# Performance work log

Measured on AMD Instinct MI355X. Metric: run time of the kernel, lower is better.

Reference implementation:

```python
import jax, jax.numpy as jnp
import numpy as np

B, D, NH, NT = 4096, 2048, 16, 4
DK = D // NH
EPS = 1e-5


def setup_inputs() -> dict:
    key = jax.random.key(0)
    ks = jax.random.split(key, 16)
    s = 0.02
    inp = {
        "e0": jax.random.normal(ks[0], (B, D), jnp.float32),
        "e1": jax.random.normal(ks[1], (B, D), jnp.float32),
        "e2": jax.random.normal(ks[2], (B, D), jnp.float32),
        "e3": jax.random.normal(ks[3], (B, D), jnp.float32),
        "quality": jax.random.uniform(ks[4], (B, NT), jnp.float32),
        "Wq": jax.random.normal(ks[5], (D, D), jnp.float32) * s,
        "bq": jnp.zeros((D,), jnp.float32),
        "Wk": jax.random.normal(ks[6], (D, D), jnp.float32) * s,
        "bk": jnp.zeros((D,), jnp.float32),
        "Wv": jax.random.normal(ks[7], (D, D), jnp.float32) * s,
        "bv": jnp.zeros((D,), jnp.float32),
        "Wo": jax.random.normal(ks[8], (D, D), jnp.float32) * s,
        "bo": jnp.zeros((D,), jnp.float32),
        "gamma": jnp.ones((D,), jnp.float32),
        "beta": jnp.zeros((D,), jnp.float32),
    }
    return inp


def _layer_norm(x, gamma, beta):
    mu = jnp.mean(x, axis=-1, keepdims=True)
    var = jnp.mean(jnp.square(x - mu), axis=-1, keepdims=True)
    return (x - mu) * jax.lax.rsqrt(var + EPS) * gamma + beta


def reference(e0, e1, e2, e3, quality, Wq, bq, Wk, bk, Wv, bv, Wo, bo, gamma, beta):
    # H: (B, T=4, D) stacked evidence representations
    H = jnp.stack([e0, e1, e2, e3], axis=1)
    # QKV projections, reshaped to (B, heads, T, dk)
    def proj(W, b):
        return (jnp.einsum('btd,ed->bte', H, W) + b).reshape(B, NT, NH, DK).transpose(0, 2, 1, 3)
    Q, K, V = proj(Wq, bq), proj(Wk, bk), proj(Wv, bv)
    # scores: (B, heads, Tq, Tk), scaled then multiplicatively quality-gated on keys
    scores = jnp.einsum('bhid,bhjd->bhij', Q, K) / jnp.sqrt(jnp.float32(DK))
    scores = scores * quality[:, None, None, :]
    attn = jax.nn.softmax(scores, axis=-1)  # dropout = identity at inference
    ctx = jnp.einsum('bhij,bhjd->bhid', attn, V)          # (B, H, T, dk)
    ctx = ctx.transpose(0, 2, 1, 3).reshape(B, NT, D)      # (B, T, D)
    ctx = jnp.einsum('btd,ed->bte', ctx, Wo) + bo
    fused = jnp.mean(ctx, axis=1)       # mean over evidence types
    residual = jnp.mean(H, axis=1)      # mean of ALL evidence types
    return _layer_norm(fused + residual, gamma, beta)
```

## Files before the change

kernel.cpp:

```cpp
#include <hip/hip_runtime.h>
#include <cstdint>
#include <cstddef>

#define BB 4096
#define DD 2048
#define NHH 16
#define NTT 4
#define DKK 128

using u16 = unsigned short;
using u32 = unsigned int;

typedef __bf16 bf16x8 __attribute__((ext_vector_type(8)));
typedef float f32x4 __attribute__((ext_vector_type(4)));

__device__ __forceinline__ float b2f(u16 u) {
    union { float f; u32 i; } c; c.i = ((u32)u) << 16; return c.f;
}
__device__ __forceinline__ u16 f2b(float f) {
    union { float f; u32 i; } c; c.f = f;
    u32 x = c.i;
    u32 r = (x + 0x7fffu + ((x >> 16) & 1u)) >> 16;
    return (u16)r;
}
__device__ __forceinline__ u32 pk(float lo, float hi) {
    u32 a = __builtin_bit_cast(u32, lo) + 0x8000u;
    u32 b = __builtin_bit_cast(u32, hi) + 0x8000u;
    return __builtin_amdgcn_perm(b, a, 0x07060302u);
}

__device__ __forceinline__ void load_lds16(const void* g, void* l) {
    __builtin_amdgcn_global_load_lds((const __attribute__((address_space(1))) void*)g,
                                     (__attribute__((address_space(3))) void*)l,
                                     16, 0, 0);
}

__global__ __launch_bounds__(256) void cvt_all(
    const float* __restrict__ e0, const float* __restrict__ e1,
    const float* __restrict__ e2, const float* __restrict__ e3,
    const float* __restrict__ Wq, const float* __restrict__ Wk,
    const float* __restrict__ Wv, const float* __restrict__ Wo,
    u16* __restrict__ Ebf, u16* __restrict__ W4, float* __restrict__ resid)
{
    const int blk = blockIdx.x;
    const int tid = threadIdx.x;
    if (blk < 4096) {
        const int b = blk;
        const int c = tid * 8;
        const size_t rb = (size_t)b * DD + c;
        const float* eps[4] = {e0, e1, e2, e3};
        float a8[8] = {0, 0, 0, 0, 0, 0, 0, 0};
#pragma unroll
        for (int t = 0; t < 4; ++t) {
            float4 p0 = *(const float4*)(eps[t] + rb);
            float4 p1 = *(const float4*)(eps[t] + rb + 4);
            u16* dst = Ebf + ((size_t)(b * 4 + t)) * DD + c;
            *(uint4*)dst = make_uint4(pk(p0.x, p0.y), pk(p0.z, p0.w),
                                      pk(p1.x, p1.y), pk(p1.z, p1.w));
            a8[0] += p0.x; a8[1] += p0.y; a8[2] += p0.z; a8[3] += p0.w;
            a8[4] += p1.x; a8[5] += p1.y; a8[6] += p1.z; a8[7] += p1.w;
        }
        *(float4*)(resid + rb)     = make_float4(a8[0] * 0.25f, a8[1] * 0.25f,
                                                 a8[2] * 0.25f, a8[3] * 0.25f);
        *(float4*)(resid + rb + 4) = make_float4(a8[4] * 0.25f, a8[5] * 0.25f,
                                                 a8[6] * 0.25f, a8[7] * 0.25f);
    } else {
        const int wb = blk - 4096;
        const int w = wb >> 11;
        const float* src = (w == 0) ? Wq : (w == 1) ? Wk : (w == 2) ? Wv : Wo;
        u16* dst = W4 + (size_t)w * DD * DD;
        const size_t i = (size_t)(wb & 2047) * 2048 + tid * 8;
        float4 a = *(const float4*)(src + i);
        float4 c2 = *(const float4*)(src + i + 4);
        *(uint4*)(dst + i) = make_uint4(pk(a.x, a.y), pk(a.z, a.w),
                                        pk(c2.x, c2.y), pk(c2.z, c2.w));
    }
}

#define QKV_COMPUTE(BI)                                                        \
    {                                                                          \
        bf16x8 af[4];                                                          \
        _Pragma("unroll")                                                      \
        for (int mi = 0; mi < 4; ++mi)                                         \
            af[mi] = *(const bf16x8*)((const char*)As[BI] +                    \
                     (wm + mi * 16 + lrow) * 64 + soff);                       \
        {                                                                      \
            bf16x8 b4[4];                                                      \
            _Pragma("unroll")                                                  \
            for (int ni = 0; ni < 4; ++ni)                                     \
                b4[ni] = *(const bf16x8*)((const char*)BQs[BI] +               \
                         (wn + ni * 16 + lrow) * 64 + soff);                   \
            _Pragma("unroll")                                                  \
            for (int mi = 0; mi < 4; ++mi)                                     \
                _Pragma("unroll")                                              \
                for (int ni = 0; ni < 4; ++ni)                                 \
                    aQ[mi][ni] = __builtin_amdgcn_mfma_f32_16x16x32_bf16(      \
                        af[mi], b4[ni], aQ[mi][ni], 0, 0, 0);                  \
        }                                                                      \
        __builtin_amdgcn_sched_barrier(0);                                     \
        {                                                                      \
            bf16x8 b4[4];                                                      \
            _Pragma("unroll")                                                  \
            for (int ni = 0; ni < 4; ++ni)                                     \
                b4[ni] = *(const bf16x8*)((const char*)BKs[BI] +               \
                         (wn + ni * 16 + lrow) * 64 + soff);                   \
            _Pragma("unroll")                                                  \
            for (int mi = 0; mi < 4; ++mi)                                     \
                _Pragma("unroll")                                              \
                for (int ni = 0; ni < 4; ++ni)                                 \
                    aK[mi][ni] = __builtin_amdgcn_mfma_f32_16x16x32_bf16(      \
                        af[mi], b4[ni], aK[mi][ni], 0, 0, 0);                  \
        }                                                                      \
        __builtin_amdgcn_sched_barrier(0);                                     \
        {                                                                      \
            bf16x8 b4[4];                                                      \
            _Pragma("unroll")                                                  \
            for (int ni = 0; ni < 4; ++ni)                                     \
                b4[ni] = *(const bf16x8*)((const char*)BVs[BI] +               \
                         (wn + ni * 16 + lrow) * 64 + soff);                   \
            _Pragma("unroll")                                                  \
            for (int mi = 0; mi < 4; ++mi)                                     \
                _Pragma("unroll")                                              \
                for (int ni = 0; ni < 4; ++ni)                                 \
                    aV[mi][ni] = __builtin_amdgcn_mfma_f32_16x16x32_bf16(      \
                        af[mi], b4[ni], aV[mi][ni], 0, 0, 0);                  \
        }                                                                      \
        __builtin_amdgcn_sched_barrier(0);                                     \
    }

#define QKV_STAGE(BI, KT)                                                      \
    {                                                                          \
        const size_t ko = (size_t)(KT) * 32;                                   \
        char* dA = (char*)As[BI]  + wave * 1024;                               \
        char* dQ = (char*)BQs[BI] + wave * 1024;                               \
        char* dK = (char*)BKs[BI] + wave * 1024;                               \
        char* dV = (char*)BVs[BI] + wave * 1024;                               \
        load_lds16(srcA + ko, dA);       load_lds16(srcA + ko + D64, dA + 4096);\
        load_lds16(srcQ + ko, dQ);       load_lds16(srcQ + ko + D64, dQ + 4096);\
        load_lds16(srcK + ko, dK);       load_lds16(srcK + ko + D64, dK + 4096);\
        load_lds16(srcV + ko, dV);       load_lds16(srcV + ko + D64, dV + 4096);\
    }

__global__ __launch_bounds__(256, 2) void qkv_attn(
    const u16* __restrict__ Ebf,
    const u16* __restrict__ Wqb, const u16* __restrict__ Wkb,
    const u16* __restrict__ Wvb,
    const float* __restrict__ bq, const float* __restrict__ bk,
    const float* __restrict__ bv, const float* __restrict__ qual,
    u16* __restrict__ ctx)
{
    __shared__ __align__(16) u16 As [2][128 * 32];
    __shared__ __align__(16) u16 BQs[2][128 * 32];
    __shared__ __align__(16) u16 BKs[2][128 * 32];
    __shared__ __align__(16) u16 BVs[2][128 * 32];
    __shared__ float exch[4][4][4][16];

    const int tid = threadIdx.x;
    const int h = blockIdx.x;
    const int m0 = blockIdx.y * 128;
    const int n0 = h * 128;

    const int wave = tid >> 6;
    const int lane = tid & 63;

    const int srow = wave * 16 + (lane >> 2);
    const int scol = ((lane & 3) ^ ((lane >> 3) & 3)) * 8;
    const u16* srcA = Ebf + (size_t)(m0 + srow) * DD + scol;
    const u16* srcQ = Wqb + (size_t)(n0 + srow) * DD + scol;
    const u16* srcK = Wkb + (size_t)(n0 + srow) * DD + scol;
    const u16* srcV = Wvb + (size_t)(n0 + srow) * DD + scol;
    const size_t D64 = (size_t)64 * DD;

    const int lrow = lane & 15;
    const int q4 = lane >> 4;
    const int wm = (wave >> 1) * 64;
    const int wn = (wave & 1) * 64;
    const int soff = (q4 ^ ((lrow >> 1) & 3)) * 16;

    f32x4 aQ[4][4] = {};
    f32x4 aK[4][4] = {};
    f32x4 aV[4][4] = {};

    QKV_STAGE(0, 0);
    __syncthreads();

#pragma unroll 1
    for (int it = 0; it < 64; it += 2) {
        QKV_STAGE(1, it + 1);
        QKV_COMPUTE(0);
        __syncthreads();
        if (it + 2 < 64) QKV_STAGE(0, it + 2);
        QKV_COMPUTE(1);
        __syncthreads();
    }

    const int quad = lane >> 4;
    const int lcol = lane & 15;

    float qb[4], kb[4], vb[4];
#pragma unroll
    for (int ni = 0; ni < 4; ++ni) {
        const int col = n0 + wn + ni * 16 + lcol;
        qb[ni] = bq[col]; kb[ni] = bk[col]; vb[ni] = bv[col];
    }

#pragma unroll
    for (int mi = 0; mi < 4; ++mi) {
        float ps[4][4];
#pragma unroll
        for (int t = 0; t < 4; ++t)
#pragma unroll
            for (int j = 0; j < 4; ++j) ps[t][j] = 0.f;

#pragma unroll
        for (int ni = 0; ni < 4; ++ni) {
            float qv[4], kv[4];
#pragma unroll
            for (int t = 0; t < 4; ++t) {
                qv[t] = aQ[mi][ni][t] + qb[ni];
                kv[t] = aK[mi][ni][t] + kb[ni];
            }
#pragma unroll
            for (int t = 0; t < 4; ++t)
#pragma unroll
                for (int j = 0; j < 4; ++j) ps[t][j] += qv[t] * kv[j];
        }
#pragma unroll
        for (int t = 0; t < 4; ++t)
#pragma unroll
            for (int j = 0; j < 4; ++j) {
                ps[t][j] += __shfl_xor(ps[t][j], 1);
                ps[t][j] += __shfl_xor(ps[t][j], 2);
                ps[t][j] += __shfl_xor(ps[t][j], 4);
                ps[t][j] += __shfl_xor(ps[t][j], 8);
            }
        if (lcol == 0) {
#pragma unroll
            for (int t = 0; t < 4; ++t)
#pragma unroll
                for (int j = 0; j < 4; ++j)
                    exch[wave][mi][quad][t * 4 + j] = ps[t][j];
        }
    }
    __syncthreads();

    const float scale = 0.08838834764831845f;
#pragma unroll
    for (int mi = 0; mi < 4; ++mi) {
        const int bbat = (m0 >> 2) + (wave >> 1) * 16 + mi * 4 + quad;

        float s16[16];
#pragma unroll
        for (int v = 0; v < 16; ++v)
            s16[v] = exch[wave][mi][quad][v] + exch[wave ^ 1][mi][quad][v];

        float qj[4];
#pragma unroll
        for (int j = 0; j < 4; ++j) qj[j] = qual[bbat * 4 + j] * scale;

        float wsum[4] = {0.f, 0.f, 0.f, 0.f};
#pragma unroll
        for (int t = 0; t < 4; ++t) {
            float sm[4]; float mx = -1e30f;
#pragma unroll
            for (int j = 0; j < 4; ++j) { sm[j] = s16[t * 4 + j] * qj[j]; mx = fmaxf(mx, sm[j]); }
            float ex[4]; float se = 0.f;
#pragma unroll
            for (int j = 0; j < 4; ++j) { ex[j] = __expf(sm[j] - mx); se += ex[j]; }
            const float inv = 0.25f / se;
#pragma unroll
            for (int j = 0; j < 4; ++j) wsum[j] += ex[j] * inv;
        }

#pragma unroll
        for (int ni = 0; ni < 4; ++ni) {
            const int col = n0 + wn + ni * 16 + lcol;
            float r = wsum[0] * aV[mi][ni][0] + wsum[1] * aV[mi][ni][1]
                    + wsum[2] * aV[mi][ni][2] + wsum[3] * aV[mi][ni][3] + vb[ni];
            ctx[(size_t)bbat * DD + col] = f2b(r);
        }
    }
}

#define O_STAGE(BI, KT)                                                        \
    {                                                                          \
        const size_t ko = (size_t)(KT) * 32;                                   \
        char* dA = (char*)As[BI] + wave * 1024;                                \
        char* dB = (char*)Bs[BI] + wave * 1024;                                \
        load_lds16(srcA + ko, dA);      load_lds16(srcA + ko + D64, dA + 4096);\
        load_lds16(srcB + ko, dB);      load_lds16(srcB + ko + D64, dB + 4096);\
    }

#define O_COMPUTE(BI)                                                          \
    {                                                                          \
        bf16x8 af[4], bfr[4];                                                  \
        _Pragma("unroll")                                                      \
        for (int i = 0; i < 4; ++i)                                            \
            af[i] = *(const bf16x8*)((const char*)As[BI] +                     \
                    (wm + i * 16 + lrow) * 64 + soff);                         \
        _Pragma("unroll")                                                      \
        for (int i = 0; i < 4; ++i)                                            \
            bfr[i] = *(const bf16x8*)((const char*)Bs[BI] +                    \
                     (wn + i * 16 + lrow) * 64 + soff);                        \
        _Pragma("unroll")                                                      \
        for (int mi = 0; mi < 4; ++mi)                                         \
            _Pragma("unroll")                                                  \
            for (int ni = 0; ni < 4; ++ni)                                     \
                acc[mi][ni] = __builtin_amdgcn_mfma_f32_16x16x32_bf16(         \
                    af[mi], bfr[ni], acc[mi][ni], 0, 0, 0);                    \
    }

__global__ __launch_bounds__(256) void o_gemm(
    const u16* __restrict__ A, const u16* __restrict__ W,
    const float* __restrict__ bia, float* __restrict__ Y)
{
    __shared__ __align__(16) u16 As[2][128 * 32];
    __shared__ __align__(16) u16 Bs[2][128 * 32];

    const int tid = threadIdx.x;
    const int m0 = blockIdx.x * 128;
    const int n0 = blockIdx.y * 128;

    const int wave = tid >> 6;
    const int lane = tid & 63;

    const int srow = wave * 16 + (lane >> 2);
    const int scol = ((lane & 3) ^ ((lane >> 3) & 3)) * 8;
    const u16* srcA = A + (size_t)(m0 + srow) * DD + scol;
    const u16* srcB = W + (size_t)(n0 + srow) * DD + scol;
    const size_t D64 = (size_t)64 * DD;

    const int wm = (wave >> 1) * 64;
    const int wn = (wave & 1) * 64;
    const int lrow = lane & 15;
    const int q4 = lane >> 4;
    const int soff = (q4 ^ ((lrow >> 1) & 3)) * 16;

    f32x4 acc[4][4] = {};

    O_STAGE(0, 0);
    __syncthreads();

#pragma unroll 1
    for (int it = 0; it < 64; it += 2) {
        O_STAGE(1, it + 1);
        O_COMPUTE(0);
        __syncthreads();
        if (it + 2 < 64) O_STAGE(0, it + 2);
        O_COMPUTE(1);
        __syncthreads();
    }

#pragma unroll
    for (int mi = 0; mi < 4; ++mi) {
#pragma unroll
        for (int r = 0; r < 4; ++r) {
            const int grow = m0 + wm + mi * 16 + (lane >> 4) * 4 + r;
#pragma unroll
            for (int ni = 0; ni < 4; ++ni) {
                const int gcol = n0 + wn + ni * 16 + (lane & 15);
                Y[(size_t)grow * DD + gcol] = acc[mi][ni][r] + bia[gcol];
            }
        }
    }
}

__global__ __launch_bounds__(256) void ln_kernel(
    const float* __restrict__ Y,
    const float* __restrict__ resid,
    const float* __restrict__ gamma, const float* __restrict__ beta,
    float* __restrict__ out)
{
    const int r = blockIdx.x;
    const int tid = threadIdx.x;
    const int c = tid * 8;
    const size_t base = (size_t)r * DD + c;

    float v[8];
    {
        float4 y0 = *(const float4*)(Y + base);
        float4 y1 = *(const float4*)(Y + base + 4);
        float4 r0 = *(const float4*)(resid + base);
        float4 r1 = *(const float4*)(resid + base + 4);
        v[0] = y0.x + r0.x; v[1] = y0.y + r0.y; v[2] = y0.z + r0.z; v[3] = y0.w + r0.w;
        v[4] = y1.x + r1.x; v[5] = y1.y + r1.y; v[6] = y1.z + r1.z; v[7] = y1.w + r1.w;
    }

    float s = 0.f, sq = 0.f;
#pragma unroll
    for (int i = 0; i < 8; ++i) { s += v[i]; sq += v[i] * v[i]; }
#pragma unroll
    for (int off = 32; off >= 1; off >>= 1) {
        s += __shfl_xor(s, off);
        sq += __shfl_xor(sq, off);
    }
    __shared__ float sh[8];
    const int lane = tid & 63, wv = tid >> 6;
    if (lane == 0) { sh[wv] = s; sh[4 + wv] = sq; }
    __syncthreads();
    s = sh[0] + sh[1] + sh[2] + sh[3];
    sq = sh[4] + sh[5] + sh[6] + sh[7];

    const float invD = 1.0f / 2048.0f;
    const float mu = s * invD;
    const float rs = rsqrtf(sq * invD - mu * mu + 1e-5f);

    float4 g0 = *(const float4*)(gamma + c);
    float4 g1 = *(const float4*)(gamma + c + 4);
    float4 b0 = *(const float4*)(beta + c);
    float4 b1 = *(const float4*)(beta + c + 4);
    float gg[8] = {g0.x, g0.y, g0.z, g0.w, g1.x, g1.y, g1.z, g1.w};
    float bb[8] = {b0.x, b0.y, b0.z, b0.w, b1.x, b1.y, b1.z, b1.w};

    float o[8];
#pragma unroll
    for (int i = 0; i < 8; ++i) o[i] = (v[i] - mu) * rs * gg[i] + bb[i];
    *(float4*)(out + base)     = make_float4(o[0], o[1], o[2], o[3]);
    *(float4*)(out + base + 4) = make_float4(o[4], o[5], o[6], o[7]);
}

extern "C" void kernel_launch(void* const* d_in, const int* in_sizes, int n_in,
                              void* d_out, int out_size, void* d_ws, size_t ws_size,
                              hipStream_t stream)
{
    const float* e0   = (const float*)d_in[0];
    const float* e1   = (const float*)d_in[1];
    const float* e2   = (const float*)d_in[2];
    const float* e3   = (const float*)d_in[3];
    const float* qual = (const float*)d_in[4];
    const float* Wq   = (const float*)d_in[5];
    const float* bq   = (const float*)d_in[6];
    const float* Wk   = (const float*)d_in[7];
    const float* bk   = (const float*)d_in[8];
    const float* Wv   = (const float*)d_in[9];
    const float* bv   = (const float*)d_in[10];
    const float* Wo   = (const float*)d_in[11];
    const float* bo   = (const float*)d_in[12];
    const float* gm   = (const float*)d_in[13];
    const float* bt   = (const float*)d_in[14];

    const size_t WD = (size_t)DD * DD;
    const size_t MQ = (size_t)BB * NTT * DD;
    const size_t ED = (size_t)BB * DD;

    u16* Ebf = (u16*)d_ws;
    u16* W4  = Ebf + MQ;
    u16* ctx = W4 + 4 * WD;
    float* Y = (float*)(ctx + ED);
    float* resid = Y + ED;

    cvt_all<<<dim3(12288), 256, 0, stream>>>(e0, e1, e2, e3, Wq, Wk, Wv, Wo,
                                             Ebf, W4, resid);

    qkv_attn<<<dim3(16, 128), 256, 0, stream>>>(Ebf, W4, W4 + WD, W4 + 2 * WD,
                                                bq, bk, bv, qual, ctx);

    o_gemm<<<dim3(32, 16), 256, 0, stream>>>(ctx, W4 + 3 * WD, bo, Y);

    ln_kernel<<<dim3(4096), 256, 0, stream>>>(Y, resid, gm, bt,
                                              (float*)d_out);
}
```

Before: 686.9 us.

## Prefetch two stages ahead with partial vmcnt waits in GEMM main loops

Restructures the double-buffered K loops of the QKV and output-projection GEMMs so both LDS buffers are filled before compute starts. Each compute step waits only until the older stage's direct-to-LDS loads have landed (partial s_waitcnt vmcnt) rather than draining all outstanding loads at a full __syncthreads. The intent is to keep one stage of global loads in flight during every compute step and hide memory latency. It relies on exact per-thread load counts per stage (8 and 4) matching the stage macros, and on hand-placed barriers and sched_barriers being correct.

```diff
diff --git a/kernel.cpp b/kernel.cpp
--- a/kernel.cpp
+++ b/kernel.cpp
@@ -34,6 +34,18 @@
                                      (__attribute__((address_space(3))) void*)l,
                                      16, 0, 0);
 }
+
+#define PIPE_WAIT(N) do {                                                      \
+    asm volatile("s_waitcnt vmcnt(" #N ")" ::: "memory");                      \
+    __builtin_amdgcn_sched_barrier(0);                                         \
+    __builtin_amdgcn_s_barrier();                                              \
+    __builtin_amdgcn_sched_barrier(0); } while (0)
+
+#define PIPE_FLIP() do {                                                       \
+    asm volatile("s_waitcnt lgkmcnt(0)" ::: "memory");                         \
+    __builtin_amdgcn_sched_barrier(0);                                         \
+    __builtin_amdgcn_s_barrier();                                              \
+    __builtin_amdgcn_sched_barrier(0); } while (0)
 
 __global__ __launch_bounds__(256) void cvt_all(
     const float* __restrict__ e0, const float* __restrict__ e1,
@@ -182,17 +194,25 @@
     f32x4 aV[4][4] = {};
 
     QKV_STAGE(0, 0);
+    QKV_STAGE(1, 1);
+
+#pragma unroll 1
+    for (int t = 0; t < 62; t += 2) {
+        PIPE_WAIT(8);
+        QKV_COMPUTE(0);
+        PIPE_FLIP();
+        QKV_STAGE(0, t + 2);
+        PIPE_WAIT(8);
+        QKV_COMPUTE(1);
+        PIPE_FLIP();
+        QKV_STAGE(1, t + 3);
+    }
+    PIPE_WAIT(8);
+    QKV_COMPUTE(0);
+    PIPE_WAIT(0);
+    QKV_COMPUTE(1);
+
     __syncthreads();
-
-#pragma unroll 1
-    for (int it = 0; it < 64; it += 2) {
-        QKV_STAGE(1, it + 1);
-        QKV_COMPUTE(0);
-        __syncthreads();
-        if (it + 2 < 64) QKV_STAGE(0, it + 2);
-        QKV_COMPUTE(1);
-        __syncthreads();
-    }
 
     const int quad = lane >> 4;
     const int lcol = lane & 15;
@@ -339,17 +359,23 @@
     f32x4 acc[4][4] = {};
 
     O_STAGE(0, 0);
-    __syncthreads();
+    O_STAGE(1, 1);
 
 #pragma unroll 1
-    for (int it = 0; it < 64; it += 2) {
-        O_STAGE(1, it + 1);
+    for (int t = 0; t < 62; t += 2) {
+        PIPE_WAIT(4);
         O_COMPUTE(0);
-        __syncthreads();
-        if (it + 2 < 64) O_STAGE(0, it + 2);
+        PIPE_FLIP();
+        O_STAGE(0, t + 2);
+        PIPE_WAIT(4);
         O_COMPUTE(1);
-        __syncthreads();
-    }
+        PIPE_FLIP();
+        O_STAGE(1, t + 3);
+    }
+    PIPE_WAIT(4);
+    O_COMPUTE(0);
+    PIPE_WAIT(0);
+    O_COMPUTE(1);
 
 #pragma unroll
     for (int mi = 0; mi < 4; ++mi) {
```

After: 664.7 us. 3.2% less time.
